# Optimization experiments

Measured on AMD Instinct MI355X. Metric: run time of the kernel, lower is better.

## Reference

```python
import jax, jax.numpy as jnp
import numpy as np

NUM_HEADS = 16
NUM_KV_HEADS = 4
HEAD_DIM = 128
EPS = 1e-6


def _rotate_half(x):
    x1, x2 = jnp.split(x, 2, axis=-1)
    return jnp.concatenate((-x2, x1), axis=-1)


def _rms_norm(x, w):
    var = jnp.mean(x * x, axis=-1, keepdims=True)
    return x * jax.lax.rsqrt(var + EPS) * w


def setup_inputs() -> dict:
    key = jax.random.key(0)
    ks = jax.random.split(key, 6)
    B, S, H = 2, 2048, 2048
    hidden_states = jax.random.normal(ks[0], (B, S, H), dtype=jnp.float32)
    # real RoPE tables (HF-style: freqs tiled twice along last dim)
    inv_freq = 1.0 / (10000.0 ** (np.arange(0, HEAD_DIM, 2, dtype=np.float32) / HEAD_DIM))
    pos = np.arange(S, dtype=np.float32)
    ang = np.concatenate([pos[:, None] * inv_freq[None, :]] * 2, axis=-1)  # [S, head_dim]
    cos = jnp.broadcast_to(jnp.cos(ang)[None], (B, S, HEAD_DIM)).astype(jnp.float32)
    sin = jnp.broadcast_to(jnp.sin(ang)[None], (B, S, HEAD_DIM)).astype(jnp.float32)
    sc = 0.02
    Wq = jax.random.normal(ks[1], (NUM_HEADS * HEAD_DIM, H), dtype=jnp.float32) * sc
    Wk = jax.random.normal(ks[2], (NUM_KV_HEADS * HEAD_DIM, H), dtype=jnp.float32) * sc
    Wv = jax.random.normal(ks[3], (NUM_KV_HEADS * HEAD_DIM, H), dtype=jnp.float32) * sc
    Wo = jax.random.normal(ks[4], (H, NUM_HEADS * HEAD_DIM), dtype=jnp.float32) * sc
    q_norm_w = jnp.ones((HEAD_DIM,), dtype=jnp.float32)
    k_norm_w = jnp.ones((HEAD_DIM,), dtype=jnp.float32)
    return {"hidden_states": hidden_states, "cos": cos, "sin": sin,
            "Wq": Wq, "Wk": Wk, "Wv": Wv, "Wo": Wo,
            "q_norm_w": q_norm_w, "k_norm_w": k_norm_w}


def reference(hidden_states, cos, sin, Wq, Wk, Wv, Wo, q_norm_w, k_norm_w):
    B, S, H = hidden_states.shape
    groups = NUM_HEADS // NUM_KV_HEADS
    # projections (Linear: x @ W^T), then [B, h, S, d]
    q = (hidden_states @ Wq.T).reshape(B, S, NUM_HEADS, HEAD_DIM).transpose(0, 2, 1, 3)
    k = (hidden_states @ Wk.T).reshape(B, S, NUM_KV_HEADS, HEAD_DIM).transpose(0, 2, 1, 3)
    v = (hidden_states @ Wv.T).reshape(B, S, NUM_KV_HEADS, HEAD_DIM).transpose(0, 2, 1, 3)
    # per-head RMSNorm
    q = _rms_norm(q, q_norm_w)
    k = _rms_norm(k, k_norm_w)
    # RoPE, cos/sin broadcast over heads (unsqueeze_dim=1)
    c = cos[:, None, :, :]
    s = sin[:, None, :, :]
    q = q * c + _rotate_half(q) * s
    k = k * c + _rotate_half(k) * s
    # GQA: expand kv heads
    k = jnp.repeat(k, groups, axis=1)
    v = jnp.repeat(v, groups, axis=1)
    scale = 1.0 / jnp.sqrt(jnp.float32(HEAD_DIM))
    scores = jnp.einsum('bhqd,bhkd->bhqk', q, k) * scale
    attn = jax.nn.softmax(scores, axis=-1)
    out = jnp.einsum('bhqk,bhkd->bhqd', attn, v)
    out = out.transpose(0, 2, 1, 3).reshape(B, S, NUM_HEADS * HEAD_DIM)
    return out @ Wo.T
```

## Files before the change

### kernel.cpp

```cpp
#include <hip/hip_runtime.h>
#include <hip/hip_bf16.h>
#include <stdint.h>

typedef __attribute__((ext_vector_type(8))) short short8;
typedef __attribute__((ext_vector_type(4))) float floatx4;
typedef __attribute__((ext_vector_type(16))) float floatx16;

#define MFMA16(a, b, c) __builtin_amdgcn_mfma_f32_16x16x32_bf16(a, b, c, 0, 0, 0)
#define MFMA32(a, b, c) __builtin_amdgcn_mfma_f32_32x32x16_bf16(a, b, c, 0, 0, 0)

static __device__ __forceinline__ void gload_lds16(const __hip_bfloat16* g, __hip_bfloat16* l) {
  __builtin_amdgcn_global_load_lds(
      (const __attribute__((address_space(1))) void*)g,
      (__attribute__((address_space(3))) void*)l,
      16, 0, 0);
}

__global__ __launch_bounds__(256)
void f2bf_all(const float* __restrict__ h, const float* __restrict__ wq,
              const float* __restrict__ wk, const float* __restrict__ wv,
              const float* __restrict__ wo, __hip_bfloat16* __restrict__ hb,
              __hip_bfloat16* __restrict__ wqkv, __hip_bfloat16* __restrict__ wob) {
  const int blk = blockIdx.x;
  const float* src;
  __hip_bfloat16* dst;
  int off;
  if (blk < 8192)       { src = h;  dst = hb;                          off = blk; }
  else if (blk < 12288) { src = wq; dst = wqkv;                        off = blk - 8192; }
  else if (blk < 13312) { src = wk; dst = wqkv + (size_t)2048 * 2048;  off = blk - 12288; }
  else if (blk < 14336) { src = wv; dst = wqkv + (size_t)2560 * 2048;  off = blk - 13312; }
  else                  { src = wo; dst = wob;                         off = blk - 14336; }
  const int i = off * 1024 + threadIdx.x * 4;
  const float4 v = *(const float4*)(src + i);
  __hip_bfloat16 t[4] = {__float2bfloat16(v.x), __float2bfloat16(v.y),
                         __float2bfloat16(v.z), __float2bfloat16(v.w)};
  *(short4*)(dst + i) = *(const short4*)t;
}

template <typename OUT_T>
__global__ __launch_bounds__(256)
void gemm_bt(const __hip_bfloat16* __restrict__ A, const __hip_bfloat16* __restrict__ Bt,
             OUT_T* __restrict__ C, int M, int N, int K) {
  __shared__ __hip_bfloat16 As[2][128 * 32];
  __shared__ __hip_bfloat16 Bs[2][128 * 32];
  const int tid = threadIdx.x;
  const int wid = tid >> 6, lane = tid & 63;
  const int lg = lane >> 4, lr = lane & 15;
  const int wr = wid >> 1, wc = wid & 1;
  const int m0 = blockIdx.x * 128, n0 = blockIdx.y * 128;
  const int nk = K >> 5;

  floatx4 acc[4][4];
#pragma unroll
  for (int mi = 0; mi < 4; ++mi)
#pragma unroll
    for (int ni = 0; ni < 4; ++ni) acc[mi][ni] = (floatx4)(0.0f);

  auto stage = [&](int buf, int kt) {
    const int k0 = kt << 5;
#pragma unroll
    for (int i = 0; i < 2; ++i) {
      const int e = (i * 256 + tid) * 8;
      const int row = e >> 5, col = e & 31;
      gload_lds16(A + (size_t)(m0 + row) * K + k0 + col, &As[buf][e]);
    }
#pragma unroll
    for (int i = 0; i < 2; ++i) {
      const int e = (i * 256 + tid) * 8;
      const int row = e >> 5, col = e & 31;
      gload_lds16(Bt + (size_t)(n0 + row) * K + k0 + col, &Bs[buf][e]);
    }
  };

  stage(0, 0);
  __syncthreads();

  for (int kt = 0; kt < nk; ++kt) {
    const int cur = kt & 1;
    if (kt + 1 < nk) stage(cur ^ 1, kt + 1);
    short8 af[4], bfr[4];
#pragma unroll
    for (int mi = 0; mi < 4; ++mi)
      af[mi] = *(const short8*)&As[cur][(wr * 64 + mi * 16 + lr) * 32 + lg * 8];
#pragma unroll
    for (int ni = 0; ni < 4; ++ni)
      bfr[ni] = *(const short8*)&Bs[cur][(wc * 64 + ni * 16 + lr) * 32 + lg * 8];
#pragma unroll
    for (int mi = 0; mi < 4; ++mi)
#pragma unroll
      for (int ni = 0; ni < 4; ++ni) acc[mi][ni] = MFMA16(af[mi], bfr[ni], acc[mi][ni]);
    __syncthreads();
  }

#pragma unroll
  for (int mi = 0; mi < 4; ++mi)
#pragma unroll
    for (int ni = 0; ni < 4; ++ni) {
      const int row = m0 + wr * 64 + mi * 16 + lg * 4;
      const int col = n0 + wc * 64 + ni * 16 + lr;
#pragma unroll
      for (int r = 0; r < 4; ++r) {
        C[(size_t)(row + r) * N + col] = (OUT_T)acc[mi][ni][r];
      }
    }
}

__global__ __launch_bounds__(256)
void normrope(const __hip_bfloat16* __restrict__ qkv, const float* __restrict__ cosb,
              const float* __restrict__ sinb, const float* __restrict__ qw,
              const float* __restrict__ kw, __hip_bfloat16* __restrict__ Q,
              __hip_bfloat16* __restrict__ Kblk) {
  const int m = blockIdx.x;
  const int b = m >> 11, s = m & 2047;
  const int wid = threadIdx.x >> 6, lane = threadIdx.x & 63;
  const size_t qkvrow = (size_t)m * 3072;
  const float c1 = cosb[(size_t)m * 128 + lane], s1 = sinb[(size_t)m * 128 + lane];
  const float c2 = cosb[(size_t)m * 128 + lane + 64], s2 = sinb[(size_t)m * 128 + lane + 64];
  const float QS = 0.12753102497113446f;
  for (int h = wid * 5; h < wid * 5 + 5; ++h) {
    const float x1 = __bfloat162float(qkv[qkvrow + h * 128 + lane]);
    const float x2 = __bfloat162float(qkv[qkvrow + h * 128 + lane + 64]);
    float ss = x1 * x1 + x2 * x2;
    ss += __shfl_xor(ss, 1);  ss += __shfl_xor(ss, 2);  ss += __shfl_xor(ss, 4);
    ss += __shfl_xor(ss, 8);  ss += __shfl_xor(ss, 16); ss += __shfl_xor(ss, 32);
    const float rs = rsqrtf(ss * (1.0f / 128.0f) + 1e-6f);
    const float* w = (h < 16) ? qw : kw;
    const float n1 = x1 * rs * w[lane], n2 = x2 * rs * w[lane + 64];
    const float o1 = n1 * c1 - n2 * s1;
    const float o2 = n2 * c2 + n1 * s2;
    if (h < 16) {
      const size_t base = ((size_t)(b * 16 + h) * 2048 + s) * 128;
      Q[base + lane] = __float2bfloat16(o1 * QS);
      Q[base + lane + 64] = __float2bfloat16(o2 * QS);
    } else {
      const int z = b * 4 + (h - 16);
      const int t = s >> 5, kv = s & 31;
      const size_t base =
          (size_t)z * 262144 + t * 4096 + (lane >> 3) * 256 + kv * 8 + (lane & 7);
      Kblk[base] = __float2bfloat16(o1);
      Kblk[base + 2048] = __float2bfloat16(o2);
    }
  }
}

__global__ __launch_bounds__(256)
void vtrans2(const __hip_bfloat16* __restrict__ qkv, __hip_bfloat16* __restrict__ Vt2) {
  __shared__ short L[64 * 65];
  const int tid = threadIdx.x;
  const int t = blockIdx.x, d0 = blockIdx.y * 64, z = blockIdx.z;
  const int b = z >> 2, hkv = z & 3;
  const int s0 = t * 64;
#pragma unroll
  for (int i = 0; i < 2; ++i) {
    const int slot = i * 256 + tid;
    const int srow = slot >> 3, c8 = (slot & 7) * 8;
    const short8 v = *(const short8*)((const short*)qkv +
        (size_t)(b * 2048 + s0 + srow) * 3072 + 2560 + hkv * 128 + d0 + c8);
#pragma unroll
    for (int j = 0; j < 8; ++j) L[(c8 + j) * 65 + srow] = v[j];
  }
  __syncthreads();
  short* dst = (short*)Vt2 + (size_t)z * 262144 + t * 8192;
#pragma unroll
  for (int i = 0; i < 2; ++i) {
    const int slot = i * 256 + tid;
    const int drow = slot >> 3, sc8 = (slot & 7) * 8;
    short8 o;
#pragma unroll
    for (int j = 0; j < 8; ++j) {
      const int p = sc8 + j;
      const int pb = p & 31;
      const int phys = (pb & 3) + ((pb >> 2) & 1) * 8 + ((pb >> 3) & 1) * 4 + (pb & 16);
      o[j] = L[drow * 65 + (p & 32) + phys];
    }
    const int addr = (sc8 >> 5) * 4096 + ((sc8 & 31) >> 3) * 1024 + (d0 + drow) * 8;
    *(short8*)&dst[addr] = o;
  }
}

__global__ __launch_bounds__(256, 3)
void fattn(const __hip_bfloat16* __restrict__ Qg, const __hip_bfloat16* __restrict__ Kb2,
           const __hip_bfloat16* __restrict__ Vt2, __hip_bfloat16* __restrict__ Og) {
  __shared__ short SMEM[17408];

  const int tid = threadIdx.x, wid = tid >> 6, lane = tid & 63;
  const int l31 = lane & 31, hi = lane >> 5;
  const int qt = blockIdx.x, bh = blockIdx.y;
  const int b = bh >> 4, h = bh & 15, hkv = h >> 2;
  const int z = b * 4 + hkv;
  const int q0w = qt * 128 + wid * 32;

  const __hip_bfloat16* Qrow = Qg + ((size_t)((b * 16 + h) * 2048 + q0w + l31)) * 128;
  short8 qf2[8];
#pragma unroll
  for (int ks = 0; ks < 8; ++ks) qf2[ks] = *(const short8*)(Qrow + ks * 16 + hi * 8);

  const short* Kbase = (const short*)Kb2 + (size_t)z * 262144;
  const short* Vbase = (const short*)Vt2 + (size_t)z * 262144;

  auto stageK = [&](int buf, int t) {
    const short* ks = Kbase + t * 4096 + tid * 8;
    short* kd = &SMEM[buf * 4096 + tid * 8];
    gload_lds16((const __hip_bfloat16*)ks, (__hip_bfloat16*)kd);
    gload_lds16((const __hip_bfloat16*)(ks + 2048), (__hip_bfloat16*)(kd + 2048));
  };
  auto stageV = [&](int buf, int t) {
    const short* vs = Vbase + t * 4096 + tid * 8;
    short* vd = &SMEM[8192 + buf * 4096 + tid * 8];
    gload_lds16((const __hip_bfloat16*)vs, (__hip_bfloat16*)vd);
    gload_lds16((const __hip_bfloat16*)(vs + 2048), (__hip_bfloat16*)(vd + 2048));
  };

  floatx16 oacc[4];
#pragma unroll
  for (int dblk = 0; dblk < 4; ++dblk) oacc[dblk] = (floatx16)(0.0f);
  float la0 = 0.0f, la1 = 0.0f;

  int pkA[8], pkB[8];

  auto doQK = [&](int kbuf, floatx16& st) {
    const short* Kt = &SMEM[kbuf * 4096];
    st = (floatx16)(0.0f);
    __builtin_amdgcn_s_setprio(1);
#pragma unroll
    for (int ks = 0; ks < 8; ++ks) {
      const short8 kf = *(const short8*)&Kt[(2 * ks + hi) * 256 + l31 * 8];
      st = MFMA32(kf, qf2[ks], st);
    }
    __builtin_amdgcn_s_setprio(0);
  };
  auto doExp = [&](const floatx16& st, int (&pk)[8]) {
#pragma unroll
    for (int m = 0; m < 8; ++m) {
      const float e0 = exp2f(st[2 * m]);
      const float e1 = exp2f(st[2 * m + 1]);
      if (m & 1) la1 += e0 + e1; else la0 += e0 + e1;
      asm("v_cvt_pk_bf16_f32 %0, %1, %2" : "=v"(pk[m]) : "v"(e0), "v"(e1));
    }
  };
  auto doPV = [&](int vbuf, const int (&pk)[8]) {
    const short* Vt = &SMEM[8192 + vbuf * 4096];
#pragma unroll
    for (int s = 0; s < 2; ++s) {
      union { int i[4]; short8 s8; } u;
      u.i[0] = pk[4 * s + 0];
      u.i[1] = pk[4 * s + 1];
      u.i[2] = pk[4 * s + 2];
      u.i[3] = pk[4 * s + 3];
      const short8 pB = u.s8;
      const int c = s * 2 + hi;
      __builtin_amdgcn_s_setprio(1);
#pragma unroll
      for (int dblk = 0; dblk < 4; ++dblk) {
        const short8 vf = *(const short8*)&Vt[c * 1024 + dblk * 256 + l31 * 8];
        oacc[dblk] = MFMA32(vf, pB, oacc[dblk]);
      }
      __builtin_amdgcn_s_setprio(0);
    }
  };

  auto body = [&](int (&pkPrev)[8], int (&pkCur)[8], int u) {
    if (u + 1 < 64) stageK((u + 1) & 1, u + 1);
    stageV(u & 1, u);
    floatx16 st;
    doQK(u & 1, st);
    doPV((u - 1) & 1, pkPrev);
    doExp(st, pkCur);
    asm volatile("s_waitcnt vmcnt(0)" ::: "memory");
    __builtin_amdgcn_s_barrier();
    __builtin_amdgcn_sched_barrier(0);
  };

  stageK(0, 0);
  asm volatile("s_waitcnt vmcnt(0)" ::: "memory");
  __builtin_amdgcn_s_barrier();
  __builtin_amdgcn_sched_barrier(0);
  {
    stageK(1, 1);
    stageV(0, 0);
    floatx16 st;
    doQK(0, st);
    doExp(st, pkA);
    asm volatile("s_waitcnt vmcnt(0)" ::: "memory");
    __builtin_amdgcn_s_barrier();
    __builtin_amdgcn_sched_barrier(0);
  }

  for (int u = 1; u < 63; u += 2) {
    body(pkA, pkB, u);
    body(pkB, pkA, u + 1);
  }
  body(pkA, pkB, 63);
  doPV(1, pkB);

  asm volatile("s_waitcnt lgkmcnt(0)" ::: "memory");
  __builtin_amdgcn_s_barrier();

  const float l_own = la0 + la1;
  const float l = l_own + __shfl_xor(l_own, 32);
  const float inv = 1.0f / l;
  short* tw = &SMEM[wid * 4352];
#pragma unroll
  for (int dblk = 0; dblk < 4; ++dblk)
#pragma unroll
    for (int a = 0; a < 4; ++a) {
      __hip_bfloat16 o4[4];
#pragma unroll
      for (int r = 0; r < 4; ++r) o4[r] = __float2bfloat16(oacc[dblk][4 * a + r] * inv);
      *(short4*)&tw[l31 * 136 + dblk * 32 + a * 8 + hi * 4] = *(const short4*)o4;
    }
  __hip_bfloat16* orow =
      Og + ((size_t)(b * 2048 + q0w + (lane >> 1))) * 2048 + h * 128 + (lane & 1) * 64;
  const short* trow = &tw[(lane >> 1) * 136 + (lane & 1) * 64];
#pragma unroll
  for (int c = 0; c < 8; ++c) {
    *(short8*)(orow + c * 8) = *(const short8*)(trow + c * 8);
  }
}

extern "C" void kernel_launch(void* const* d_in, const int* in_sizes, int n_in,
                              void* d_out, int out_size, void* d_ws, size_t ws_size,
                              hipStream_t stream) {
  const float* hidden = (const float*)d_in[0];
  const float* cosb = (const float*)d_in[1];
  const float* sinb = (const float*)d_in[2];
  const float* Wq = (const float*)d_in[3];
  const float* Wk = (const float*)d_in[4];
  const float* Wv = (const float*)d_in[5];
  const float* Wo = (const float*)d_in[6];
  const float* qw = (const float*)d_in[7];
  const float* kw = (const float*)d_in[8];

  char* ws = (char*)d_ws;
  __hip_bfloat16* hidden_bf = (__hip_bfloat16*)ws; ws += (size_t)4096 * 2048 * 2;
  __hip_bfloat16* wqkv = (__hip_bfloat16*)ws;      ws += (size_t)3072 * 2048 * 2;
  __hip_bfloat16* wo_bf = (__hip_bfloat16*)ws;     ws += (size_t)2048 * 2048 * 2;
  __hip_bfloat16* qkv = (__hip_bfloat16*)ws;       ws += (size_t)4096 * 3072 * 2;
  __hip_bfloat16* Qb = (__hip_bfloat16*)ws;        ws += (size_t)2 * 16 * 2048 * 128 * 2;
  __hip_bfloat16* Kblk = (__hip_bfloat16*)ws;      ws += (size_t)2 * 4 * 2048 * 128 * 2;
  __hip_bfloat16* attn = (__hip_bfloat16*)ws;      ws += (size_t)4096 * 2048 * 2;
  __hip_bfloat16* Vt2 = wqkv;

  f2bf_all<<<18432, 256, 0, stream>>>(hidden, Wq, Wk, Wv, Wo, hidden_bf, wqkv, wo_bf);

  gemm_bt<__hip_bfloat16><<<dim3(32, 24), 256, 0, stream>>>(hidden_bf, wqkv, qkv, 4096, 3072, 2048);
  normrope<<<4096, 256, 0, stream>>>(qkv, cosb, sinb, qw, kw, Qb, Kblk);
  vtrans2<<<dim3(32, 2, 8), 256, 0, stream>>>(qkv, Vt2);
  fattn<<<dim3(16, 32), 256, 0, stream>>>(Qb, Kblk, Vt2, attn);
  gemm_bt<float><<<dim3(32, 16), 256, 0, stream>>>(attn, wo_bf, (float*)d_out, 4096, 2048, 2048);
}
```

Before: 230.7 us.

## Use pre-blocked operand layout and 256x256-tile GEMM for QKV projection

The fp32-to-bf16 conversion now writes hidden states and the QKV weights in a fragment-blocked layout (16-row by 32-col units matching the MFMA operand order) and handles 8 elements per thread. A new 512-thread GEMM kernel with 256x256 tiles loads these blocks straight into LDS via global_load_lds and reads MFMA fragments without address swizzling. It uses a split-k double-buffered pipeline with raised wave priority during the MFMAs. This aims to raise arithmetic intensity and cut LDS address overhead in the QKV projection. The costs are one block per CU, only 192 blocks, and a layout coupling that other kernels reading wqkv must respect.

After: 238.6 us. +3.4%, slower.

```diff
diff --git a/kernel.cpp b/kernel.cpp
--- a/kernel.cpp
+++ b/kernel.cpp
@@ -24,17 +24,115 @@
   const int blk = blockIdx.x;
   const float* src;
   __hip_bfloat16* dst;
-  int off;
-  if (blk < 8192)       { src = h;  dst = hb;                          off = blk; }
-  else if (blk < 12288) { src = wq; dst = wqkv;                        off = blk - 8192; }
-  else if (blk < 13312) { src = wk; dst = wqkv + (size_t)2048 * 2048;  off = blk - 12288; }
-  else if (blk < 14336) { src = wv; dst = wqkv + (size_t)2560 * 2048;  off = blk - 13312; }
-  else                  { src = wo; dst = wob;                         off = blk - 14336; }
-  const int i = off * 1024 + threadIdx.x * 4;
-  const float4 v = *(const float4*)(src + i);
-  __hip_bfloat16 t[4] = {__float2bfloat16(v.x), __float2bfloat16(v.y),
-                         __float2bfloat16(v.z), __float2bfloat16(v.w)};
-  *(short4*)(dst + i) = *(const short4*)t;
+  int off, rowoff, blocked;
+  if (blk < 4096)      { src = h;  dst = hb;   off = blk;        rowoff = 0;    blocked = 1; }
+  else if (blk < 6144) { src = wq; dst = wqkv; off = blk - 4096; rowoff = 0;    blocked = 1; }
+  else if (blk < 6656) { src = wk; dst = wqkv; off = blk - 6144; rowoff = 2048; blocked = 1; }
+  else if (blk < 7168) { src = wv; dst = wqkv; off = blk - 6656; rowoff = 2560; blocked = 1; }
+  else                 { src = wo; dst = wob;  off = blk - 7168; rowoff = 0;    blocked = 0; }
+  const int E = off * 2048 + threadIdx.x * 8;
+  const float4 a = *(const float4*)(src + E);
+  const float4 b = *(const float4*)(src + E + 4);
+  __hip_bfloat16 t[8] = {__float2bfloat16(a.x), __float2bfloat16(a.y),
+                         __float2bfloat16(a.z), __float2bfloat16(a.w),
+                         __float2bfloat16(b.x), __float2bfloat16(b.y),
+                         __float2bfloat16(b.z), __float2bfloat16(b.w)};
+  size_t o;
+  if (blocked) {
+    const int row = rowoff + (E >> 11), col = E & 2047;
+    const int u = (row >> 4) * 64 + (col >> 5);
+    const int l = (row & 15) + (((col >> 3) & 3) << 4);
+    o = (size_t)u * 512 + l * 8;
+  } else {
+    o = (size_t)E;
+  }
+  *(short8*)((short*)dst + o) = *(const short8*)t;
+}
+
+template <typename OUT_T>
+__global__ __launch_bounds__(512, 1)
+void gemm8(const __hip_bfloat16* __restrict__ Ab, const __hip_bfloat16* __restrict__ Bb,
+           OUT_T* __restrict__ C, int M, int N) {
+  __shared__ short SMEM[2][32768];
+
+  const int tid = threadIdx.x, wid = tid >> 6, lane = tid & 63;
+  const int lg = lane >> 4, lr = lane & 15;
+  const int wr = wid >> 2, wc = wid & 3;
+  const int m0 = blockIdx.x * 256, n0 = blockIdx.y * 256;
+
+  const short* A = (const short*)Ab;
+  const short* B = (const short*)Bb;
+
+  floatx4 acc[8][4];
+#pragma unroll
+  for (int mi = 0; mi < 8; ++mi)
+#pragma unroll
+    for (int ni = 0; ni < 4; ++ni) acc[mi][ni] = (floatx4)(0.0f);
+
+  auto stage_half = [&](int buf, int t, int ks) {
+    const int ksg = t * 2 + ks;
+#pragma unroll
+    for (int j = 0; j < 2; ++j) {
+      const int ub = wid * 2 + j;
+      gload_lds16((const __hip_bfloat16*)(A + (((size_t)(m0 >> 4) + ub) * 64 + ksg) * 512 + lane * 8),
+                  (__hip_bfloat16*)(&SMEM[buf][(ks * 16 + ub) * 512 + lane * 8]));
+      gload_lds16((const __hip_bfloat16*)(B + (((size_t)(n0 >> 4) + ub) * 64 + ksg) * 512 + lane * 8),
+                  (__hip_bfloat16*)(&SMEM[buf][16384 + (ks * 16 + ub) * 512 + lane * 8]));
+    }
+  };
+
+  auto compute_ks = [&](int buf, int ks) {
+    const short* base = &SMEM[buf][ks * 16 * 512];
+    short8 af[8], bf[4];
+#pragma unroll
+    for (int mi = 0; mi < 8; ++mi)
+      af[mi] = *(const short8*)&base[(wr * 8 + mi) * 512 + lane * 8];
+#pragma unroll
+    for (int ni = 0; ni < 4; ++ni)
+      bf[ni] = *(const short8*)&base[16384 + (wc * 4 + ni) * 512 + lane * 8];
+    __builtin_amdgcn_s_setprio(1);
+#pragma unroll
+    for (int mi = 0; mi < 8; ++mi)
+#pragma unroll
+      for (int ni = 0; ni < 4; ++ni) acc[mi][ni] = MFMA16(af[mi], bf[ni], acc[mi][ni]);
+    __builtin_amdgcn_s_setprio(0);
+  };
+
+  stage_half(0, 0, 0);
+  stage_half(0, 0, 1);
+  stage_half(1, 1, 0);
+  asm volatile("s_waitcnt vmcnt(4)" ::: "memory");
+  __builtin_amdgcn_s_barrier();
+  __builtin_amdgcn_sched_barrier(0);
+
+  for (int t = 0; t < 32; ++t) {
+    const int X = t & 1;
+    if (t + 1 < 32) stage_half(X ^ 1, t + 1, 1);
+    compute_ks(X, 0);
+    __builtin_amdgcn_s_barrier();
+    __builtin_amdgcn_sched_barrier(0);
+    if (t + 2 < 32) stage_half(X, t + 2, 0);
+    compute_ks(X, 1);
+    if (t + 2 < 32) {
+      asm volatile("s_waitcnt vmcnt(4)" ::: "memory");
+    } else {
+      asm volatile("s_waitcnt vmcnt(0)" ::: "memory");
+    }
+    __builtin_amdgcn_s_barrier();
+    __builtin_amdgcn_sched_barrier(0);
+  }
+
+#pragma unroll
+  for (int mi = 0; mi < 8; ++mi)
+#pragma unroll
+    for (int ni = 0; ni < 4; ++ni) {
+      const int row = m0 + wr * 128 + mi * 16 + lg * 4;
+      const int col = n0 + wc * 64 + ni * 16 + lr;
+#pragma unroll
+      for (int r = 0; r < 4; ++r) {
+        C[(size_t)(row + r) * N + col] = (OUT_T)acc[mi][ni][r];
+      }
+    }
 }
 
 template <typename OUT_T>
@@ -341,9 +439,9 @@
   __hip_bfloat16* attn = (__hip_bfloat16*)ws;      ws += (size_t)4096 * 2048 * 2;
   __hip_bfloat16* Vt2 = wqkv;
 
-  f2bf_all<<<18432, 256, 0, stream>>>(hidden, Wq, Wk, Wv, Wo, hidden_bf, wqkv, wo_bf);
-
-  gemm_bt<__hip_bfloat16><<<dim3(32, 24), 256, 0, stream>>>(hidden_bf, wqkv, qkv, 4096, 3072, 2048);
+  f2bf_all<<<9216, 256, 0, stream>>>(hidden, Wq, Wk, Wv, Wo, hidden_bf, wqkv, wo_bf);
+
+  gemm8<__hip_bfloat16><<<dim3(16, 12), 512, 0, stream>>>(hidden_bf, wqkv, qkv, 4096, 3072);
   normrope<<<4096, 256, 0, stream>>>(qkv, cosb, sinb, qw, kw, Qb, Kblk);
   vtrans2<<<dim3(32, 2, 8), 256, 0, stream>>>(qkv, Vt2);
   fattn<<<dim3(16, 32), 256, 0, stream>>>(Qb, Kblk, Vt2, attn);
```

## Triple-buffer GEMM LDS staging with XOR swizzle and explicit vmcnt waits

Applied to the files above, without the earlier changes.

Replaces the GEMM's double-buffered LDS tiles with a three-stage ring, so global-to-LDS loads run two k-steps ahead of the MFMA compute. Manual s_waitcnt/s_barrier calls replace __syncthreads. The change also XOR-swizzles the 16-byte column groups in LDS to reduce bank conflicts on the fragment reads. In exchange it uses more LDS per block, which may lower occupancy, and it depends on hand-counted vmcnt values being correct.

After: 267.2 us. +15.8%, slower.

```diff
diff --git a/kernel.cpp b/kernel.cpp
--- a/kernel.cpp
+++ b/kernel.cpp
@@ -41,8 +41,8 @@
 __global__ __launch_bounds__(256)
 void gemm_bt(const __hip_bfloat16* __restrict__ A, const __hip_bfloat16* __restrict__ Bt,
              OUT_T* __restrict__ C, int M, int N, int K) {
-  __shared__ __hip_bfloat16 As[2][128 * 32];
-  __shared__ __hip_bfloat16 Bs[2][128 * 32];
+  __shared__ short LDS[3 * 8192];
+
   const int tid = threadIdx.x;
   const int wid = tid >> 6, lane = tid & 63;
   const int lg = lane >> 4, lr = lane & 15;
@@ -50,6 +50,8 @@
   const int m0 = blockIdx.x * 128, n0 = blockIdx.y * 128;
   const int nk = K >> 5;
 
+  const int axor = (lg ^ ((lr >> 1) & 3)) * 8;
+
   floatx4 acc[4][4];
 #pragma unroll
   for (int mi = 0; mi < 4; ++mi)
@@ -58,38 +60,60 @@
 
   auto stage = [&](int buf, int kt) {
     const int k0 = kt << 5;
+    short* dst = &LDS[buf * 8192];
 #pragma unroll
     for (int i = 0; i < 2; ++i) {
-      const int e = (i * 256 + tid) * 8;
-      const int row = e >> 5, col = e & 31;
-      gload_lds16(A + (size_t)(m0 + row) * K + k0 + col, &As[buf][e]);
+      const int c = i * 256 + tid;
+      const int row = c >> 2;
+      const int gp = (c & 3) ^ ((row >> 1) & 3);
+      gload_lds16(A + (size_t)(m0 + row) * K + k0 + gp * 8, (__hip_bfloat16*)(dst + c * 8));
     }
 #pragma unroll
     for (int i = 0; i < 2; ++i) {
-      const int e = (i * 256 + tid) * 8;
-      const int row = e >> 5, col = e & 31;
-      gload_lds16(Bt + (size_t)(n0 + row) * K + k0 + col, &Bs[buf][e]);
-    }
+      const int c = i * 256 + tid;
+      const int row = c >> 2;
+      const int gp = (c & 3) ^ ((row >> 1) & 3);
+      gload_lds16(Bt + (size_t)(n0 + row) * K + k0 + gp * 8,
+                  (__hip_bfloat16*)(dst + 4096 + c * 8));
+    }
+  };
+
+  auto compute = [&](int buf) {
+    const short* base = &LDS[buf * 8192];
+    short8 af[4], bfr[4];
+#pragma unroll
+    for (int mi = 0; mi < 4; ++mi) {
+      const int row = wr * 64 + mi * 16 + lr;
+      af[mi] = *(const short8*)&base[row * 32 + axor];
+    }
+#pragma unroll
+    for (int ni = 0; ni < 4; ++ni) {
+      const int row = wc * 64 + ni * 16 + lr;
+      bfr[ni] = *(const short8*)&base[4096 + row * 32 + axor];
+    }
+#pragma unroll
+    for (int mi = 0; mi < 4; ++mi)
+#pragma unroll
+      for (int ni = 0; ni < 4; ++ni) acc[mi][ni] = MFMA16(af[mi], bfr[ni], acc[mi][ni]);
   };
 
   stage(0, 0);
-  __syncthreads();
+  stage(1, 1);
+  asm volatile("s_waitcnt vmcnt(4)" ::: "memory");
+  __builtin_amdgcn_s_barrier();
+  __builtin_amdgcn_sched_barrier(0);
 
   for (int kt = 0; kt < nk; ++kt) {
-    const int cur = kt & 1;
-    if (kt + 1 < nk) stage(cur ^ 1, kt + 1);
-    short8 af[4], bfr[4];
-#pragma unroll
-    for (int mi = 0; mi < 4; ++mi)
-      af[mi] = *(const short8*)&As[cur][(wr * 64 + mi * 16 + lr) * 32 + lg * 8];
-#pragma unroll
-    for (int ni = 0; ni < 4; ++ni)
-      bfr[ni] = *(const short8*)&Bs[cur][(wc * 64 + ni * 16 + lr) * 32 + lg * 8];
-#pragma unroll
-    for (int mi = 0; mi < 4; ++mi)
-#pragma unroll
-      for (int ni = 0; ni < 4; ++ni) acc[mi][ni] = MFMA16(af[mi], bfr[ni], acc[mi][ni]);
-    __syncthreads();
+    if (kt + 2 < nk) {
+      stage((kt + 2) % 3, kt + 2);
+      compute(kt % 3);
+      asm volatile("s_waitcnt vmcnt(4)" ::: "memory");
+    } else {
+      compute(kt % 3);
+      asm volatile("s_waitcnt vmcnt(0)" ::: "memory");
+    }
+    __builtin_amdgcn_s_barrier();
+    __builtin_amdgcn_sched_barrier(0);
   }
 
 #pragma unroll
```
